# Kernel optimization log

Measured on AMD Instinct MI355X. Metric: run time of the kernel, lower is better.

## Reference

```python
import jax, jax.numpy as jnp
import numpy as np

N_NODES = 10000
N_EDGES = 200000
M = 16           # env_embed_mul (channels)
HD = 16          # head_dim
LAT = 128        # latent dim
NODE_INV = 64
EDGE_INV = 32
ISQRTD = 4       # math.isqrt(HD) -- source MULTIPLIES scores by this (faithful)
INV_SQRT3 = float(1.0 / np.sqrt(3.0))  # normalized CG for 1o x 1o -> 0e


def _layer_norm(x, g, b, eps=1e-5):
    mu = jnp.mean(x, axis=-1, keepdims=True)
    var = jnp.mean((x - mu) ** 2, axis=-1, keepdims=True)
    return (x - mu) * jax.lax.rsqrt(var + eps) * g + b


def _weight_channels(x, w):
    # MakeWeightedChannels: x [E,4] = (0e,1o) SH; w [E, M*2] per-irrep per-channel weights -> [E,M,4]
    w = w.reshape(-1, M, 2)
    s = x[:, None, 0:1] * w[:, :, 0:1]
    v = x[:, None, 1:4] * w[:, :, 1:2]
    return jnp.concatenate([s, v], axis=-1)


def _scatter_softmax(w, seg, num_segments):
    m = jax.lax.stop_gradient(jax.ops.segment_max(w, seg, num_segments=num_segments))
    m = jnp.where(jnp.isfinite(m), m, 0.0)
    ex = jnp.exp(w - m[seg])
    den = jax.ops.segment_sum(ex, seg, num_segments=num_segments)
    return ex / jnp.maximum(den[seg], 1e-30)


def setup_inputs() -> dict:
    key = jax.random.key(0)
    ks = iter(jax.random.split(key, 48))
    def nrm(shape, scale=1.0):
        return jax.random.normal(next(ks), shape, dtype=jnp.float32) * np.float32(scale)
    D_in = 2 * NODE_INV + EDGE_INV  # 160
    GENW = 2 * (M * 2) + M          # 80
    inp = {}
    inp['latents'] = jnp.zeros((N_EDGES, LAT), jnp.float32)
    inp['inv_latent_cat'] = nrm((N_EDGES, D_in))
    inp['eq_features'] = nrm((N_EDGES, 4))
    inp['cutoff_coeffs'] = jax.random.uniform(next(ks), (N_EDGES,), dtype=jnp.float32)
    inp['edge_attr'] = nrm((N_EDGES, 4))
    inp['node_invariants'] = nrm((N_NODES, NODE_INV))
    inp['edge_invariants'] = nrm((N_EDGES, EDGE_INV))
    # two-body latent MLP (layer 0)
    inp['W1'] = nrm((D_in, LAT), 1.0 / np.sqrt(D_in)); inp['b1'] = jnp.zeros((LAT,), jnp.float32)
    inp['W2'] = nrm((LAT, LAT), 1.0 / np.sqrt(LAT));   inp['b2'] = jnp.zeros((LAT,), jnp.float32)
    # env_embed MLP + LayerNorm
    inp['Wenv'] = nrm((LAT, GENW), 1.0 / np.sqrt(LAT)); inp['benv'] = jnp.zeros((GENW,), jnp.float32)
    inp['ln_g'] = jnp.ones((GENW,), jnp.float32); inp['ln_b'] = jnp.zeros((GENW,), jnp.float32)
    # attention query (LN + linear)
    inp['lnq_g'] = jnp.ones((D_in,), jnp.float32); inp['lnq_b'] = jnp.zeros((D_in,), jnp.float32)
    inp['Wq'] = nrm((D_in, M * HD), 1.0 / np.sqrt(D_in)); inp['bq'] = jnp.zeros((M * HD,), jnp.float32)
    # FullyConnectedTensorProduct -> Mx0e (two paths: 0e x 0e, 1o x 1o)
    inp['Wd1'] = nrm((M, M, M), 1.0 / M)
    inp['Wd2'] = nrm((M, M, M), 1.0 / M)
    # attention key (LN + linear)
    inp['lnk_g'] = jnp.ones((M,), jnp.float32); inp['lnk_b'] = jnp.zeros((M,), jnp.float32)
    inp['Wk'] = nrm((M, M * HD), 1.0 / np.sqrt(M)); inp['bk'] = jnp.zeros((M * HD,), jnp.float32)
    # env_linear (per-irrep channel mixing)
    inp['Ws'] = nrm((M, M), 1.0 / np.sqrt(M))
    inp['Wv'] = nrm((M, M), 1.0 / np.sqrt(M))
    # output e3nn Linear: 2 scalar blocks -> M scalars, 2 vector blocks -> M vectors
    inp['Wls'] = nrm((2 * M, M), 1.0 / np.sqrt(2 * M))
    inp['Wlv'] = nrm((2 * M, M), 1.0 / np.sqrt(2 * M))
    inp['active_edges'] = jnp.arange(N_EDGES, dtype=jnp.int32)
    inp['edge_center'] = jax.random.randint(next(ks), (N_EDGES,), 0, N_NODES)
    inp['edge_neighbor'] = jax.random.randint(next(ks), (N_EDGES,), 0, N_NODES)
    inp['num_nodes'] = N_NODES
    return inp


def reference(latents, inv_latent_cat, eq_features, cutoff_coeffs, edge_attr,
              node_invariants, edge_invariants,
              W1, b1, W2, b2, Wenv, benv, ln_g, ln_b,
              lnq_g, lnq_b, Wq, bq, Wd1, Wd2, lnk_g, lnk_b, Wk, bk,
              Ws, Wv, Wls, Wlv,
              active_edges, edge_center, edge_neighbor, num_nodes):
    # --- two-body latent MLP (layer_index == 0), cutoff gating, index_copy ---
    h = jax.nn.silu(inv_latent_cat @ W1 + b1)
    new_latents = (h @ W2 + b2) * cutoff_coeffs[:, None]
    latents = latents.at[active_edges].set(new_latents)
    lat_act = latents[active_edges]                               # [E, LAT]
    # --- env_embed MLP + LayerNorm -> per-edge generated weights ---
    weights = _layer_norm(lat_act @ Wenv + benv, ln_g, ln_b)      # [E, 80]
    wn = M * 2
    eqf = _weight_channels(eq_features, weights[:, :wn])          # [E, M, 4]
    emb = _weight_channels(edge_attr, weights[:, wn:2 * wn])      # [E, M, 4]
    # --- per-edge multi-channel attention ---
    efa = jnp.concatenate([node_invariants[edge_center],
                           node_invariants[edge_neighbor],
                           edge_invariants], axis=-1)             # [E, 160]
    Q = (_layer_norm(efa, lnq_g, lnq_b) @ Wq + bq).reshape(-1, M, HD)
    s1, v1 = emb[:, :, 0], emb[:, :, 1:]
    s2, v2 = eqf[:, :, 0], eqf[:, :, 1:]
    # FullyConnectedTensorProduct(env, env -> Mx0e)
    dot = (jnp.einsum('eu,ev,uvw->ew', s1, s2, Wd1)
           + INV_SQRT3 * jnp.einsum('eui,evi,uvw->ew', v1, v2, Wd2))
    K = (_layer_norm(dot, lnk_g, lnk_b) @ Wk + bk).reshape(-1, M, HD)
    Wa = jnp.einsum('emd,emd->em', Q, K) * ISQRTD
    attn = _scatter_softmax(Wa, edge_center, num_nodes)           # [E, M]
    emb = emb * attn[:, :, None]
    # --- neighbor aggregation (scatter-sum over edge centers) ---
    env = jax.ops.segment_sum(emb, edge_center, num_segments=num_nodes)  # [N, M, 4]
    # env_linear: per-irrep channel mixing (inactive nodes are all-zero, never read)
    env = jnp.concatenate([
        jnp.einsum('nu,uw->nw', env[:, :, 0], Ws)[:, :, None],
        jnp.einsum('nui,uw->nwi', env[:, :, 1:], Wv)], axis=-1)
    env_e = env[edge_center]                                      # [E, M, 4]
    # --- Contracter (uuu, channelwise CG TP, (0e+1o) x (0e+1o)) ---
    a_s, a_v = eqf[:, :, 0:1], eqf[:, :, 1:]
    b_s, b_v = env_e[:, :, 0:1], env_e[:, :, 1:]
    tp = jnp.concatenate([
        a_s * b_s,                                                # 0e x 0e -> 0e
        INV_SQRT3 * jnp.sum(a_v * b_v, axis=-1, keepdims=True),   # 1o x 1o -> 0e
        a_s * b_v,                                                # 0e x 1o -> 1o
        a_v * b_s], axis=-1)                                      # 1o x 0e -> 1o  [E, M, 8]
    scalars = tp[:, :, :2].reshape(-1, 2 * M)                     # 'e m s -> e (m s)'
    inv_latent = jnp.concatenate([lat_act, scalars], axis=-1)     # [E, LAT + 2M]
    # --- output Linear over full_out_irreps ---
    s_out = tp[:, :, :2].reshape(-1, 2 * M) @ Wls                 # [E, M]
    v_out = jnp.einsum('eui,uw->ewi', tp[:, :, 2:].reshape(-1, 2 * M, 3), Wlv)
    eq_out = jnp.concatenate([s_out[:, :, None], v_out], axis=-1) # [E, M, 4]
    return (latents, inv_latent, eq_out)
```

## Files before the change

### kernel.cpp

```cpp
#include <hip/hip_runtime.h>
#include <hip/hip_bf16.h>

#define EDGES 200000
#define NN    10000
#define DIN   160
#define LATD  128
#define GENW  80
#define M     16
#define NODEINV 64
#define EDGEINV 32
#define INV_SQRT3F 0.57735026918962576f

__device__ __forceinline__ unsigned fkey(float x){ unsigned u=__float_as_uint(x); return (u&0x80000000u)? ~u : (u|0x80000000u); }
__device__ __forceinline__ float  unfkey(unsigned k){ unsigned u=(k&0x80000000u)? (k&0x7fffffffu) : ~k; return __uint_as_float(u); }
__device__ __forceinline__ void atomAddF(float* p, float v){
  __hip_atomic_fetch_add(p, v, __ATOMIC_RELAXED, __HIP_MEMORY_SCOPE_AGENT);
}

__global__ __launch_bounds__(256) void k_mlp1(const float* __restrict__ X, const float* __restrict__ W1,
                                              const float* __restrict__ b1, float* __restrict__ hout){
  long e = (long)blockIdx.x*256 + threadIdx.x;
  if (e >= EDGES) return;
  const float* x = X + e*DIN;
  for (int jb = 0; jb < LATD; jb += 16){
    float acc[16];
    #pragma unroll
    for (int j=0;j<16;j++) acc[j] = b1[jb+j];
    for (int k=0;k<DIN;k++){
      float xk = x[k];
      const float* wr = W1 + (long)k*LATD + jb;
      #pragma unroll
      for (int j=0;j<16;j++) acc[j] = fmaf(xk, wr[j], acc[j]);
    }
    #pragma unroll
    for (int j=0;j<16;j++){
      float a = acc[j];
      hout[e*LATD + jb + j] = a / (1.0f + __expf(-a));
    }
  }
}

__global__ __launch_bounds__(256) void k_mlp2(const float* __restrict__ hbuf, const float* __restrict__ W2,
    const float* __restrict__ b2, const float* __restrict__ cutoff,
    const float* __restrict__ Wenv, const float* __restrict__ benv,
    const float* __restrict__ ln_g, const float* __restrict__ ln_b,
    const int* __restrict__ active,
    float* __restrict__ out0, float* __restrict__ w64){
  long e = (long)blockIdx.x*256 + threadIdx.x;
  if (e >= EDGES) return;
  const float* h = hbuf + e*LATD;
  float co = cutoff[e];
  float p[GENW];
  #pragma unroll
  for (int w=0;w<GENW;w++) p[w] = benv[w];
  long   ae = active[e];
  float* lat_row = out0 + ae*LATD;
  for (int jb=0;jb<LATD;jb+=16){
    float acc[16];
    #pragma unroll
    for (int j=0;j<16;j++) acc[j] = b2[jb+j];
    for (int k=0;k<LATD;k++){
      float hk = h[k];
      const float* wr = W2 + (long)k*LATD + jb;
      #pragma unroll
      for (int j=0;j<16;j++) acc[j] = fmaf(hk, wr[j], acc[j]);
    }
    #pragma unroll
    for (int j=0;j<16;j++){
      float l = acc[j]*co;
      lat_row[jb+j] = l;
      const float* we = Wenv + (long)(jb+j)*GENW;
      #pragma unroll
      for (int w=0;w<GENW;w++) p[w] = fmaf(l, we[w], p[w]);
    }
  }
  float s = 0.f;
  #pragma unroll
  for (int w=0;w<GENW;w++) s += p[w];
  float mu = s*(1.0f/GENW);
  float v = 0.f;
  #pragma unroll
  for (int w=0;w<GENW;w++){ float d = p[w]-mu; v += d*d; }
  float rstd = rsqrtf(v*(1.0f/GENW) + 1e-5f);
  float* wrow = w64 + e*64;
  #pragma unroll
  for (int w=0;w<64;w++)
    wrow[w] = (p[w]-mu)*rstd*ln_g[w] + ln_b[w];
}

__global__ __launch_bounds__(256) void k_qk(
  const float* __restrict__ node_inv, const float* __restrict__ edge_inv,
  const float* __restrict__ eq_feat,  const float* __restrict__ edge_attr,
  const int* __restrict__ ecen, const int* __restrict__ enei,
  const float* __restrict__ w64,
  const float* __restrict__ lnq_g, const float* __restrict__ lnq_b,
  const float* __restrict__ Wq, const float* __restrict__ bq,
  const float* __restrict__ Wd1, const float* __restrict__ Wd2,
  const float* __restrict__ lnk_g, const float* __restrict__ lnk_b,
  const float* __restrict__ Wk, const float* __restrict__ bk,
  float* __restrict__ waOut)
{
  long e = (long)blockIdx.x*256 + threadIdx.x;
  if (e >= EDGES) return;

  const float* ea = edge_attr + e*4;
  const float* ef = eq_feat  + e*4;
  float ea0=ea[0], ea1=ea[1], ea2=ea[2], ea3=ea[3];
  float ef0=ef[0], ef1=ef[1], ef2=ef[2], ef3=ef[3];
  float cf = INV_SQRT3F*(ea1*ef1 + ea2*ef2 + ea3*ef3);

  float aU[M], bU[M], sE[M], sC[M];
  {
    const float* wrow = w64 + e*64;
    #pragma unroll
    for (int m=0;m<M;m++){
      sE[m] = ef0*wrow[2*m];
      sC[m] = wrow[2*m+1];
      aU[m] = ea0*wrow[32+2*m];
      bU[m] = cf *wrow[33+2*m];
    }
  }
  float dotv[16];
  #pragma unroll
  for (int w=0;w<16;w++) dotv[w]=0.f;
  for (int u=0;u<M;u++){
    float au = aU[u], bu = bU[u];
    for (int v=0;v<M;v++){
      float a = au*sE[v];
      float b = bu*sC[v];
      const float* d1 = Wd1 + (u*M+v)*M;
      const float* d2 = Wd2 + (u*M+v)*M;
      #pragma unroll
      for (int w=0;w<16;w++) dotv[w] += a*d1[w] + b*d2[w];
    }
  }
  float ds=0.f;
  #pragma unroll
  for (int w=0;w<16;w++) ds += dotv[w];
  float dmu = ds*(1.0f/16.0f);
  float dvar=0.f;
  #pragma unroll
  for (int w=0;w<16;w++){ float d=dotv[w]-dmu; dvar += d*d; }
  float drstd = rsqrtf(dvar*(1.0f/16.0f) + 1e-5f);
  float lnv[16];
  #pragma unroll
  for (int u=0;u<16;u++) lnv[u] = (dotv[u]-dmu)*drstd*lnk_g[u] + lnk_b[u];

  int c = ecen[e], nb = enei[e];
  const float* nc = node_inv + (long)c*NODEINV;
  const float* nn = node_inv + (long)nb*NODEINV;
  const float* ei = edge_inv + e*EDGEINV;
  float s1=0.f, s2=0.f;
  for (int k=0;k<NODEINV;k++){ float a=nc[k]; s1+=a; s2+=a*a; }
  for (int k=0;k<NODEINV;k++){ float a=nn[k]; s1+=a; s2+=a*a; }
  for (int k=0;k<EDGEINV;k++){ float a=ei[k]; s1+=a; s2+=a*a; }
  float mu   = s1*(1.0f/DIN);
  float rstd = rsqrtf(s2*(1.0f/DIN) - mu*mu + 1e-5f);

  for (int m=0;m<M;m++){
    float q[16];
    #pragma unroll
    for (int d=0;d<16;d++) q[d] = bq[m*16+d];
    for (int k=0;k<NODEINV;k++){
      float x = (nc[k]-mu)*rstd*lnq_g[k] + lnq_b[k];
      const float* wr = Wq + (long)k*256 + m*16;
      #pragma unroll
      for (int d=0;d<16;d++) q[d] = fmaf(x, wr[d], q[d]);
    }
    for (int k=0;k<NODEINV;k++){
      float x = (nn[k]-mu)*rstd*lnq_g[64+k] + lnq_b[64+k];
      const float* wr = Wq + (long)(64+k)*256 + m*16;
      #pragma unroll
      for (int d=0;d<16;d++) q[d] = fmaf(x, wr[d], q[d]);
    }
    for (int k=0;k<EDGEINV;k++){
      float x = (ei[k]-mu)*rstd*lnq_g[128+k] + lnq_b[128+k];
      const float* wr = Wq + (long)(128+k)*256 + m*16;
      #pragma unroll
      for (int d=0;d<16;d++) q[d] = fmaf(x, wr[d], q[d]);
    }
    float kk[16];
    #pragma unroll
    for (int d=0;d<16;d++) kk[d] = bk[m*16+d];
    #pragma unroll
    for (int u=0;u<16;u++){
      const float* wr = Wk + u*256 + m*16;
      float lu = lnv[u];
      #pragma unroll
      for (int d=0;d<16;d++) kk[d] = fmaf(lu, wr[d], kk[d]);
    }
    float wa = 0.f;
    #pragma unroll
    for (int d=0;d<16;d++) wa += q[d]*kk[d];
    waOut[e*16+m] = 4.0f * wa;
  }
}

__global__ __launch_bounds__(256) void k_amax(const float* __restrict__ wa, const int* __restrict__ ecen,
                                              unsigned* __restrict__ nmax){
  long e = (long)blockIdx.x*256 + threadIdx.x;
  if (e >= EDGES) return;
  int c = ecen[e];
  for (int m=0;m<M;m++) atomicMax(&nmax[c*16+m], fkey(wa[e*16+m]));
}

__global__ __launch_bounds__(256) void k_den(const float* __restrict__ wa, const int* __restrict__ ecen,
                                             const unsigned* __restrict__ nmax, float* __restrict__ nden){
  long e = (long)blockIdx.x*256 + threadIdx.x;
  if (e >= EDGES) return;
  int c = ecen[e];
  for (int m=0;m<M;m++){
    float mx = unfkey(nmax[c*16+m]);
    atomAddF(&nden[c*16+m], __expf(wa[e*16+m] - mx));
  }
}

__global__ __launch_bounds__(256) void k_env(const float* __restrict__ wa, const unsigned* __restrict__ nmax,
    const float* __restrict__ nden, const int* __restrict__ ecen, const float* __restrict__ edge_attr,
    const float* __restrict__ w64, float* __restrict__ envacc){
  long e = (long)blockIdx.x*256 + threadIdx.x;
  if (e >= EDGES) return;
  int c = ecen[e];
  const float* wrow = w64 + e*64;
  const float* ea = edge_attr + e*4;
  float ea0=ea[0], ea1=ea[1], ea2=ea[2], ea3=ea[3];
  for (int m=0;m<M;m++){
    float mx   = unfkey(nmax[c*16+m]);
    float attn = __expf(wa[e*16+m] - mx) / fmaxf(nden[c*16+m], 1e-30f);
    float wA = wrow[32+2*m] * attn;
    float wB = wrow[33+2*m] * attn;
    float* dst = envacc + ((long)c*16+m)*4;
    atomAddF(dst+0, ea0*wA);
    atomAddF(dst+1, ea1*wB);
    atomAddF(dst+2, ea2*wB);
    atomAddF(dst+3, ea3*wB);
  }
}

__global__ __launch_bounds__(256) void k_envmix(const float* __restrict__ env, const float* __restrict__ Ws,
                                                const float* __restrict__ Wv, float* __restrict__ envm){
  long n = (long)blockIdx.x*256 + threadIdx.x;
  if (n >= NN) return;
  float accs[16], accv[16][3];
  #pragma unroll
  for (int w=0;w<16;w++){ accs[w]=0.f; accv[w][0]=0.f; accv[w][1]=0.f; accv[w][2]=0.f; }
  for (int u=0;u<M;u++){
    const float* er = env + (n*16+u)*4;
    float e0=er[0], e1=er[1], e2=er[2], e3=er[3];
    #pragma unroll
    for (int w=0;w<16;w++){
      float ws = Ws[u*16+w], wv = Wv[u*16+w];
      accs[w]    = fmaf(e0, ws, accs[w]);
      accv[w][0] = fmaf(e1, wv, accv[w][0]);
      accv[w][1] = fmaf(e2, wv, accv[w][1]);
      accv[w][2] = fmaf(e3, wv, accv[w][2]);
    }
  }
  float* o = envm + n*64;
  #pragma unroll
  for (int w=0;w<16;w++){
    o[w*4+0]=accs[w]; o[w*4+1]=accv[w][0]; o[w*4+2]=accv[w][1]; o[w*4+3]=accv[w][2];
  }
}

__global__ __launch_bounds__(256) void k_final(const float* __restrict__ eq_feat,
    const int* __restrict__ ecen, const int* __restrict__ active,
    const float* __restrict__ out0, const float* __restrict__ envm,
    const float* __restrict__ w64,
    const float* __restrict__ Wls, const float* __restrict__ Wlv,
    float* __restrict__ out1, float* __restrict__ out2){
  long e = (long)blockIdx.x*256 + threadIdx.x;
  if (e >= EDGES) return;
  int c = ecen[e];
  long ae = active[e];
  {
    const float4* src = (const float4*)(out0 + ae*LATD);
    float4* dst = (float4*)(out1 + e*DIN);
    #pragma unroll
    for (int j=0;j<32;j++) dst[j] = src[j];
  }
  const float* wrow = w64 + e*64;
  const float* ee = envm + (long)c*64;
  const float* ef = eq_feat + e*4;
  float ef0=ef[0], ef1=ef[1], ef2=ef[2], ef3=ef[3];
  float sacc[16], vacc[16][3];
  #pragma unroll
  for (int w=0;w<16;w++){ sacc[w]=0.f; vacc[w][0]=0.f; vacc[w][1]=0.f; vacc[w][2]=0.f; }
  float* inv_sc = out1 + e*DIN + 128;
  for (int m=0;m<M;m++){
    float wE = wrow[2*m], wC = wrow[2*m+1];
    float as_ = ef0*wE;
    float av0 = ef1*wC, av1 = ef2*wC, av2 = ef3*wC;
    float bs_ = ee[m*4+0], bv0 = ee[m*4+1], bv1 = ee[m*4+2], bv2 = ee[m*4+3];
    float t0 = as_*bs_;
    float t1 = INV_SQRT3F*(av0*bv0 + av1*bv1 + av2*bv2);
    inv_sc[2*m]   = t0;
    inv_sc[2*m+1] = t1;
    const float* l0 = Wls + (2*m)*16; const float* l1 = l0 + 16;
    const float* v0 = Wlv + (2*m)*16; const float* v1 = v0 + 16;
    float p0 = as_*bv0, p1 = as_*bv1, p2 = as_*bv2;
    float r0 = av0*bs_, r1 = av1*bs_, r2 = av2*bs_;
    #pragma unroll
    for (int w=0;w<16;w++){
      sacc[w]    += t0*l0[w] + t1*l1[w];
      vacc[w][0] += p0*v0[w] + r0*v1[w];
      vacc[w][1] += p1*v0[w] + r1*v1[w];
      vacc[w][2] += p2*v0[w] + r2*v1[w];
    }
  }
  float* o2 = out2 + e*64;
  #pragma unroll
  for (int w=0;w<16;w++){
    o2[w*4+0]=sacc[w]; o2[w*4+1]=vacc[w][0]; o2[w*4+2]=vacc[w][1]; o2[w*4+3]=vacc[w][2];
  }
}

extern "C" void kernel_launch(void* const* d_in, const int* in_sizes, int n_in,
                              void* d_out, int out_size, void* d_ws, size_t ws_size,
                              hipStream_t stream) {
  (void)in_sizes; (void)n_in; (void)out_size; (void)ws_size;
  const float* latents_in = (const float*)d_in[0]; (void)latents_in;
  const float* inv_cat    = (const float*)d_in[1];
  const float* eq_feat    = (const float*)d_in[2];
  const float* cutoff     = (const float*)d_in[3];
  const float* edge_attr  = (const float*)d_in[4];
  const float* node_inv   = (const float*)d_in[5];
  const float* edge_inv   = (const float*)d_in[6];
  const float* W1   = (const float*)d_in[7];
  const float* b1   = (const float*)d_in[8];
  const float* W2   = (const float*)d_in[9];
  const float* b2   = (const float*)d_in[10];
  const float* Wenv = (const float*)d_in[11];
  const float* benv = (const float*)d_in[12];
  const float* ln_g = (const float*)d_in[13];
  const float* ln_b = (const float*)d_in[14];
  const float* lnq_g= (const float*)d_in[15];
  const float* lnq_b= (const float*)d_in[16];
  const float* Wq   = (const float*)d_in[17];
  const float* bq   = (const float*)d_in[18];
  const float* Wd1  = (const float*)d_in[19];
  const float* Wd2  = (const float*)d_in[20];
  const float* lnk_g= (const float*)d_in[21];
  const float* lnk_b= (const float*)d_in[22];
  const float* Wk   = (const float*)d_in[23];
  const float* bk   = (const float*)d_in[24];
  const float* Ws_  = (const float*)d_in[25];
  const float* Wv_  = (const float*)d_in[26];
  const float* Wls  = (const float*)d_in[27];
  const float* Wlv  = (const float*)d_in[28];
  const int* active = (const int*)d_in[29];
  const int* ecen   = (const int*)d_in[30];
  const int* enei   = (const int*)d_in[31];

  float* out0 = (float*)d_out;
  float* out1 = out0 + (long)EDGES*LATD;
  float* out2 = out1 + (long)EDGES*DIN;
  float* ws_h = out1;

  char* ws = (char*)d_ws;
  float*    ws_w64  = (float*)(ws + 0);
  float*    ws_wa   = (float*)(ws + 51200000);
  unsigned* ws_nmax = (unsigned*)(ws + 64000000);
  float*    ws_nden = (float*)(ws + 64640000);
  float*    ws_env  = (float*)(ws + 65280000);
  float*    ws_envm = (float*)(ws + 67840000);

  hipMemsetAsync(ws + 64000000, 0, 640000 + 640000 + 2560000, stream);

  const int gE = (EDGES + 255) / 256;
  k_mlp1<<<gE, 256, 0, stream>>>(inv_cat, W1, b1, ws_h);
  k_mlp2<<<gE, 256, 0, stream>>>(ws_h, W2, b2, cutoff, Wenv, benv, ln_g, ln_b, active, out0, ws_w64);
  k_qk<<<gE, 256, 0, stream>>>(node_inv, edge_inv, eq_feat, edge_attr, ecen, enei, ws_w64,
                               lnq_g, lnq_b, Wq, bq, Wd1, Wd2, lnk_g, lnk_b, Wk, bk, ws_wa);
  k_amax<<<gE, 256, 0, stream>>>(ws_wa, ecen, ws_nmax);
  k_den<<<gE, 256, 0, stream>>>(ws_wa, ecen, ws_nmax, ws_nden);
  k_env<<<gE, 256, 0, stream>>>(ws_wa, ws_nmax, ws_nden, ecen, edge_attr, ws_w64, ws_env);
  k_envmix<<<(NN + 255)/256, 256, 0, stream>>>(ws_env, Ws_, Wv_, ws_envm);
  k_final<<<gE, 256, 0, stream>>>(eq_feat, ecen, active, out0, ws_envm, ws_w64, Wls, Wlv, out1, out2);
}
```

Measured before the change: 3.902 ms.

## Fuse MLP kernels and split per-edge work across 16 threads with LDS staging

```diff
diff --git a/kernel.cpp b/kernel.cpp
--- a/kernel.cpp
+++ b/kernel.cpp
@@ -1,5 +1,4 @@
 #include <hip/hip_runtime.h>
-#include <hip/hip_bf16.h>
 
 #define EDGES 200000
 #define NN    10000
@@ -17,75 +16,107 @@
   __hip_atomic_fetch_add(p, v, __ATOMIC_RELAXED, __HIP_MEMORY_SCOPE_AGENT);
 }
 
-__global__ __launch_bounds__(256) void k_mlp1(const float* __restrict__ X, const float* __restrict__ W1,
-                                              const float* __restrict__ b1, float* __restrict__ hout){
-  long e = (long)blockIdx.x*256 + threadIdx.x;
-  if (e >= EDGES) return;
-  const float* x = X + e*DIN;
-  for (int jb = 0; jb < LATD; jb += 16){
-    float acc[16];
-    #pragma unroll
-    for (int j=0;j<16;j++) acc[j] = b1[jb+j];
-    for (int k=0;k<DIN;k++){
-      float xk = x[k];
-      const float* wr = W1 + (long)k*LATD + jb;
-      #pragma unroll
-      for (int j=0;j<16;j++) acc[j] = fmaf(xk, wr[j], acc[j]);
-    }
-    #pragma unroll
-    for (int j=0;j<16;j++){
-      float a = acc[j];
-      hout[e*LATD + jb + j] = a / (1.0f + __expf(-a));
-    }
-  }
-}
-
-__global__ __launch_bounds__(256) void k_mlp2(const float* __restrict__ hbuf, const float* __restrict__ W2,
-    const float* __restrict__ b2, const float* __restrict__ cutoff,
+__global__ __launch_bounds__(256) void k_mlp(
+    const float* __restrict__ X,  const float* __restrict__ W1, const float* __restrict__ b1,
+    const float* __restrict__ W2, const float* __restrict__ b2,
+    const float* __restrict__ cutoff,
     const float* __restrict__ Wenv, const float* __restrict__ benv,
     const float* __restrict__ ln_g, const float* __restrict__ ln_b,
     const int* __restrict__ active,
-    float* __restrict__ out0, float* __restrict__ w64){
-  long e = (long)blockIdx.x*256 + threadIdx.x;
-  if (e >= EDGES) return;
-  const float* h = hbuf + e*LATD;
-  float co = cutoff[e];
-  float p[GENW];
-  #pragma unroll
-  for (int w=0;w<GENW;w++) p[w] = benv[w];
-  long   ae = active[e];
-  float* lat_row = out0 + ae*LATD;
-  for (int jb=0;jb<LATD;jb+=16){
-    float acc[16];
-    #pragma unroll
-    for (int j=0;j<16;j++) acc[j] = b2[jb+j];
+    float* __restrict__ out0, float* __restrict__ w64)
+{
+  __shared__ float lds_x[16][164];
+  __shared__ float lds_h[16][132];
+  __shared__ float lds_l[16][132];
+  const int tid = threadIdx.x;
+  const int eL  = tid >> 4;
+  const int m   = tid & 15;
+  const long e  = (long)blockIdx.x*16 + eL;
+
+  {
+    const float* x = X + e*DIN;
+    #pragma unroll
+    for (int i=0;i<10;i++){ int k = m + 16*i; lds_x[eL][k] = x[k]; }
+  }
+  __syncthreads();
+
+  {
+    float acc[8];
+    const float* bb = b1 + m*8;
+    #pragma unroll
+    for (int j=0;j<8;j++) acc[j] = bb[j];
+    for (int k=0;k<DIN;k++){
+      float xk = lds_x[eL][k];
+      const float* wr = W1 + (long)k*LATD + m*8;
+      float4 w0 = *(const float4*)(wr);
+      float4 w1 = *(const float4*)(wr+4);
+      acc[0]=fmaf(xk,w0.x,acc[0]); acc[1]=fmaf(xk,w0.y,acc[1]);
+      acc[2]=fmaf(xk,w0.z,acc[2]); acc[3]=fmaf(xk,w0.w,acc[3]);
+      acc[4]=fmaf(xk,w1.x,acc[4]); acc[5]=fmaf(xk,w1.y,acc[5]);
+      acc[6]=fmaf(xk,w1.z,acc[6]); acc[7]=fmaf(xk,w1.w,acc[7]);
+    }
+    #pragma unroll
+    for (int j=0;j<8;j++){
+      float a = acc[j];
+      lds_h[eL][m*8+j] = a / (1.0f + __expf(-a));
+    }
+  }
+  __syncthreads();
+
+  const float co = cutoff[e];
+  const long  ae = active[e];
+  {
+    float acc[8];
+    const float* bb = b2 + m*8;
+    #pragma unroll
+    for (int j=0;j<8;j++) acc[j] = bb[j];
     for (int k=0;k<LATD;k++){
-      float hk = h[k];
-      const float* wr = W2 + (long)k*LATD + jb;
+      float hk = lds_h[eL][k];
+      const float* wr = W2 + (long)k*LATD + m*8;
+      float4 w0 = *(const float4*)(wr);
+      float4 w1 = *(const float4*)(wr+4);
+      acc[0]=fmaf(hk,w0.x,acc[0]); acc[1]=fmaf(hk,w0.y,acc[1]);
+      acc[2]=fmaf(hk,w0.z,acc[2]); acc[3]=fmaf(hk,w0.w,acc[3]);
+      acc[4]=fmaf(hk,w1.x,acc[4]); acc[5]=fmaf(hk,w1.y,acc[5]);
+      acc[6]=fmaf(hk,w1.z,acc[6]); acc[7]=fmaf(hk,w1.w,acc[7]);
+    }
+    #pragma unroll
+    for (int j=0;j<8;j++) acc[j] *= co;
+    float4 o0 = make_float4(acc[0],acc[1],acc[2],acc[3]);
+    float4 o1 = make_float4(acc[4],acc[5],acc[6],acc[7]);
+    *(float4*)(out0 + ae*LATD + m*8)     = o0;
+    *(float4*)(out0 + ae*LATD + m*8 + 4) = o1;
+    #pragma unroll
+    for (int j=0;j<8;j++) lds_l[eL][m*8+j] = acc[j];
+  }
+  __syncthreads();
+
+  {
+    float p[5];
+    #pragma unroll
+    for (int t=0;t<5;t++) p[t] = benv[m*5+t];
+    for (int l=0;l<LATD;l++){
+      float lv = lds_l[eL][l];
+      const float* we = Wenv + (long)l*GENW + m*5;
       #pragma unroll
-      for (int j=0;j<16;j++) acc[j] = fmaf(hk, wr[j], acc[j]);
-    }
-    #pragma unroll
-    for (int j=0;j<16;j++){
-      float l = acc[j]*co;
-      lat_row[jb+j] = l;
-      const float* we = Wenv + (long)(jb+j)*GENW;
-      #pragma unroll
-      for (int w=0;w<GENW;w++) p[w] = fmaf(l, we[w], p[w]);
-    }
-  }
-  float s = 0.f;
-  #pragma unroll
-  for (int w=0;w<GENW;w++) s += p[w];
-  float mu = s*(1.0f/GENW);
-  float v = 0.f;
-  #pragma unroll
-  for (int w=0;w<GENW;w++){ float d = p[w]-mu; v += d*d; }
-  float rstd = rsqrtf(v*(1.0f/GENW) + 1e-5f);
-  float* wrow = w64 + e*64;
-  #pragma unroll
-  for (int w=0;w<64;w++)
-    wrow[w] = (p[w]-mu)*rstd*ln_g[w] + ln_b[w];
+      for (int t=0;t<5;t++) p[t] = fmaf(lv, we[t], p[t]);
+    }
+    float s1=0.f, s2=0.f;
+    #pragma unroll
+    for (int t=0;t<5;t++){ s1 += p[t]; s2 += p[t]*p[t]; }
+    #pragma unroll
+    for (int off=1; off<16; off<<=1){
+      s1 += __shfl_xor(s1, off, 16);
+      s2 += __shfl_xor(s2, off, 16);
+    }
+    float mu   = s1*(1.0f/GENW);
+    float rstd = rsqrtf(s2*(1.0f/GENW) - mu*mu + 1e-5f);
+    #pragma unroll
+    for (int t=0;t<5;t++){
+      int j = m*5+t;
+      if (j < 64) w64[e*64 + j] = (p[t]-mu)*rstd*ln_g[j] + ln_b[j];
+    }
+  }
 }
 
 __global__ __launch_bounds__(256) void k_qk(
@@ -100,100 +131,119 @@
   const float* __restrict__ Wk, const float* __restrict__ bk,
   float* __restrict__ waOut)
 {
-  long e = (long)blockIdx.x*256 + threadIdx.x;
-  if (e >= EDGES) return;
-
-  const float* ea = edge_attr + e*4;
-  const float* ef = eq_feat  + e*4;
-  float ea0=ea[0], ea1=ea[1], ea2=ea[2], ea3=ea[3];
-  float ef0=ef[0], ef1=ef[1], ef2=ef[2], ef3=ef[3];
-  float cf = INV_SQRT3F*(ea1*ef1 + ea2*ef2 + ea3*ef3);
-
-  float aU[M], bU[M], sE[M], sC[M];
-  {
-    const float* wrow = w64 + e*64;
-    #pragma unroll
-    for (int m=0;m<M;m++){
-      sE[m] = ef0*wrow[2*m];
-      sC[m] = wrow[2*m+1];
-      aU[m] = ea0*wrow[32+2*m];
-      bU[m] = cf *wrow[33+2*m];
-    }
-  }
-  float dotv[16];
-  #pragma unroll
-  for (int w=0;w<16;w++) dotv[w]=0.f;
-  for (int u=0;u<M;u++){
-    float au = aU[u], bu = bU[u];
-    for (int v=0;v<M;v++){
-      float a = au*sE[v];
-      float b = bu*sC[v];
-      const float* d1 = Wd1 + (u*M+v)*M;
-      const float* d2 = Wd2 + (u*M+v)*M;
-      #pragma unroll
-      for (int w=0;w<16;w++) dotv[w] += a*d1[w] + b*d2[w];
-    }
-  }
-  float ds=0.f;
-  #pragma unroll
-  for (int w=0;w<16;w++) ds += dotv[w];
-  float dmu = ds*(1.0f/16.0f);
-  float dvar=0.f;
-  #pragma unroll
-  for (int w=0;w<16;w++){ float d=dotv[w]-dmu; dvar += d*d; }
-  float drstd = rsqrtf(dvar*(1.0f/16.0f) + 1e-5f);
-  float lnv[16];
-  #pragma unroll
-  for (int u=0;u<16;u++) lnv[u] = (dotv[u]-dmu)*drstd*lnk_g[u] + lnk_b[u];
-
-  int c = ecen[e], nb = enei[e];
-  const float* nc = node_inv + (long)c*NODEINV;
-  const float* nn = node_inv + (long)nb*NODEINV;
-  const float* ei = edge_inv + e*EDGEINV;
+  __shared__ float lds_x[16][164];
+  __shared__ float lds_w[16][68];
+  const int tid = threadIdx.x;
+  const int eL  = tid >> 4;
+  const int m   = tid & 15;
+  const long e  = (long)blockIdx.x*16 + eL;
+
+  {
+    float4 w4 = *(const float4*)(w64 + e*64 + m*4);
+    lds_w[eL][m*4+0]=w4.x; lds_w[eL][m*4+1]=w4.y;
+    lds_w[eL][m*4+2]=w4.z; lds_w[eL][m*4+3]=w4.w;
+  }
+
+  const int c = ecen[e], nb = enei[e];
+  const float* ncp = node_inv + (long)c*NODEINV;
+  const float* nnp = node_inv + (long)nb*NODEINV;
+  const float* eip = edge_inv + e*EDGEINV;
+  float raw[10];
   float s1=0.f, s2=0.f;
-  for (int k=0;k<NODEINV;k++){ float a=nc[k]; s1+=a; s2+=a*a; }
-  for (int k=0;k<NODEINV;k++){ float a=nn[k]; s1+=a; s2+=a*a; }
-  for (int k=0;k<EDGEINV;k++){ float a=ei[k]; s1+=a; s2+=a*a; }
+  #pragma unroll
+  for (int i=0;i<10;i++){
+    int k = m + 16*i;
+    float v = (i<4)? ncp[k] : ((i<8)? nnp[k-64] : eip[k-128]);
+    raw[i]=v; s1+=v; s2+=v*v;
+  }
+  #pragma unroll
+  for (int off=1; off<16; off<<=1){
+    s1 += __shfl_xor(s1, off, 16);
+    s2 += __shfl_xor(s2, off, 16);
+  }
   float mu   = s1*(1.0f/DIN);
   float rstd = rsqrtf(s2*(1.0f/DIN) - mu*mu + 1e-5f);
-
-  for (int m=0;m<M;m++){
-    float q[16];
-    #pragma unroll
-    for (int d=0;d<16;d++) q[d] = bq[m*16+d];
-    for (int k=0;k<NODEINV;k++){
-      float x = (nc[k]-mu)*rstd*lnq_g[k] + lnq_b[k];
-      const float* wr = Wq + (long)k*256 + m*16;
-      #pragma unroll
-      for (int d=0;d<16;d++) q[d] = fmaf(x, wr[d], q[d]);
-    }
-    for (int k=0;k<NODEINV;k++){
-      float x = (nn[k]-mu)*rstd*lnq_g[64+k] + lnq_b[64+k];
-      const float* wr = Wq + (long)(64+k)*256 + m*16;
-      #pragma unroll
-      for (int d=0;d<16;d++) q[d] = fmaf(x, wr[d], q[d]);
-    }
-    for (int k=0;k<EDGEINV;k++){
-      float x = (ei[k]-mu)*rstd*lnq_g[128+k] + lnq_b[128+k];
-      const float* wr = Wq + (long)(128+k)*256 + m*16;
-      #pragma unroll
-      for (int d=0;d<16;d++) q[d] = fmaf(x, wr[d], q[d]);
-    }
-    float kk[16];
-    #pragma unroll
-    for (int d=0;d<16;d++) kk[d] = bk[m*16+d];
-    #pragma unroll
-    for (int u=0;u<16;u++){
-      const float* wr = Wk + u*256 + m*16;
-      float lu = lnv[u];
-      #pragma unroll
-      for (int d=0;d<16;d++) kk[d] = fmaf(lu, wr[d], kk[d]);
-    }
-    float wa = 0.f;
-    #pragma unroll
-    for (int d=0;d<16;d++) wa += q[d]*kk[d];
-    waOut[e*16+m] = 4.0f * wa;
-  }
+  #pragma unroll
+  for (int i=0;i<10;i++){
+    int k = m + 16*i;
+    lds_x[eL][k] = (raw[i]-mu)*rstd*lnq_g[k] + lnq_b[k];
+  }
+  __syncthreads();
+
+  float4 eav = *(const float4*)(edge_attr + e*4);
+  float4 efv = *(const float4*)(eq_feat  + e*4);
+  float cf     = INV_SQRT3F*(eav.y*efv.y + eav.z*efv.z + eav.w*efv.w);
+  float scaleA = eav.x * efv.x;
+
+  float sEv[16], sCv[16];
+  #pragma unroll
+  for (int v=0;v<16;v++){ sEv[v]=lds_w[eL][2*v]; sCv[v]=lds_w[eL][2*v+1]; }
+
+  float dotm = 0.f;
+  #pragma unroll 4
+  for (int u=0;u<16;u++){
+    float au = scaleA * lds_w[eL][32+2*u];
+    float bu = cf     * lds_w[eL][33+2*u];
+    const float* d1 = Wd1 + u*256 + m;
+    const float* d2 = Wd2 + u*256 + m;
+    float tE=0.f, tC=0.f;
+    #pragma unroll
+    for (int v=0;v<16;v++){
+      tE = fmaf(sEv[v], d1[v*16], tE);
+      tC = fmaf(sCv[v], d2[v*16], tC);
+    }
+    dotm = fmaf(au, tE, fmaf(bu, tC, dotm));
+  }
+
+  float ds1 = dotm, ds2 = dotm*dotm;
+  #pragma unroll
+  for (int off=1; off<16; off<<=1){
+    ds1 += __shfl_xor(ds1, off, 16);
+    ds2 += __shfl_xor(ds2, off, 16);
+  }
+  float dmu   = ds1*(1.0f/16.0f);
+  float drstd = rsqrtf(ds2*(1.0f/16.0f) - dmu*dmu + 1e-5f);
+  float lnvm  = (dotm-dmu)*drstd*lnk_g[m] + lnk_b[m];
+
+  float kk[16];
+  #pragma unroll
+  for (int d=0; d<16; d+=4){
+    float4 bv = *(const float4*)(bk + m*16 + d);
+    kk[d]=bv.x; kk[d+1]=bv.y; kk[d+2]=bv.z; kk[d+3]=bv.w;
+  }
+  #pragma unroll 4
+  for (int u=0;u<16;u++){
+    float lu = __shfl(lnvm, u, 16);
+    const float* wr = Wk + u*256 + m*16;
+    #pragma unroll
+    for (int d=0;d<16;d+=4){
+      float4 wv = *(const float4*)(wr + d);
+      kk[d]  =fmaf(lu,wv.x,kk[d]);   kk[d+1]=fmaf(lu,wv.y,kk[d+1]);
+      kk[d+2]=fmaf(lu,wv.z,kk[d+2]); kk[d+3]=fmaf(lu,wv.w,kk[d+3]);
+    }
+  }
+
+  float q[16];
+  #pragma unroll
+  for (int d=0; d<16; d+=4){
+    float4 bv = *(const float4*)(bq + m*16 + d);
+    q[d]=bv.x; q[d+1]=bv.y; q[d+2]=bv.z; q[d+3]=bv.w;
+  }
+  for (int k=0;k<DIN;k++){
+    float xk = lds_x[eL][k];
+    const float* wr = Wq + (long)k*256 + m*16;
+    #pragma unroll
+    for (int d=0;d<16;d+=4){
+      float4 wv = *(const float4*)(wr + d);
+      q[d]  =fmaf(xk,wv.x,q[d]);   q[d+1]=fmaf(xk,wv.y,q[d+1]);
+      q[d+2]=fmaf(xk,wv.z,q[d+2]); q[d+3]=fmaf(xk,wv.w,q[d+3]);
+    }
+  }
+
+  float wa = 0.f;
+  #pragma unroll
+  for (int d=0;d<16;d++) wa += q[d]*kk[d];
+  waOut[e*16+m] = 4.0f * wa;
 }
 
 __global__ __launch_bounds__(256) void k_amax(const float* __restrict__ wa, const int* __restrict__ ecen,
@@ -355,7 +405,6 @@
   float* out0 = (float*)d_out;
   float* out1 = out0 + (long)EDGES*LATD;
   float* out2 = out1 + (long)EDGES*DIN;
-  float* ws_h = out1;
 
   char* ws = (char*)d_ws;
   float*    ws_w64  = (float*)(ws + 0);
@@ -367,14 +416,16 @@
 
   hipMemsetAsync(ws + 64000000, 0, 640000 + 640000 + 2560000, stream);
 
-  const int gE = (EDGES + 255) / 256;
-  k_mlp1<<<gE, 256, 0, stream>>>(inv_cat, W1, b1, ws_h);
-  k_mlp2<<<gE, 256, 0, stream>>>(ws_h, W2, b2, cutoff, Wenv, benv, ln_g, ln_b, active, out0, ws_w64);
-  k_qk<<<gE, 256, 0, stream>>>(node_inv, edge_inv, eq_feat, edge_attr, ecen, enei, ws_w64,
-                               lnq_g, lnq_b, Wq, bq, Wd1, Wd2, lnk_g, lnk_b, Wk, bk, ws_wa);
+  const int gE16 = (EDGES + 15) / 16;
+  const int gE   = (EDGES + 255) / 256;
+
+  k_mlp<<<gE16, 256, 0, stream>>>(inv_cat, W1, b1, W2, b2, cutoff, Wenv, benv,
+                                  ln_g, ln_b, active, out0, ws_w64);
+  k_qk <<<gE16, 256, 0, stream>>>(node_inv, edge_inv, eq_feat, edge_attr, ecen, enei, ws_w64,
+                                  lnq_g, lnq_b, Wq, bq, Wd1, Wd2, lnk_g, lnk_b, Wk, bk, ws_wa);
   k_amax<<<gE, 256, 0, stream>>>(ws_wa, ecen, ws_nmax);
-  k_den<<<gE, 256, 0, stream>>>(ws_wa, ecen, ws_nmax, ws_nden);
-  k_env<<<gE, 256, 0, stream>>>(ws_wa, ws_nmax, ws_nden, ecen, edge_attr, ws_w64, ws_env);
+  k_den <<<gE, 256, 0, stream>>>(ws_wa, ecen, ws_nmax, ws_nden);
+  k_env <<<gE, 256, 0, stream>>>(ws_wa, ws_nmax, ws_nden, ecen, edge_attr, ws_w64, ws_env);
   k_envmix<<<(NN + 255)/256, 256, 0, stream>>>(ws_env, Ws_, Wv_, ws_envm);
   k_final<<<gE, 256, 0, stream>>>(eq_feat, ecen, active, out0, ws_envm, ws_w64, Wls, Wlv, out1, out2);
 }
```

Result: slower. 5.156 ms (+32.1%).
